# Performance work log

Measured on AMD Instinct MI355X. Metric: run time of the kernel, lower is better.

Reference implementation:

```python
import jax, jax.numpy as jnp
import numpy as np
from jax import lax

B, S, H, E, K = 2, 1024, 2048, 16, 4
CAP = int(B * S * 1.5 * K / E)  # capacity = 768
ALPHA = 0.7

def _mlp2(x, w1, b1, w2, b2):
    return jnp.maximum(x @ w1 + b1, 0.0) @ w2 + b2

def setup_inputs() -> dict:
    key = jax.random.key(0)
    ks = iter(jax.random.split(key, 32))
    def w(shape, scale=0.02):
        return (jax.random.normal(next(ks), shape, dtype=jnp.float32) * scale)
    inp = {
        'hidden_states': jax.random.normal(next(ks), (B, S, H), dtype=jnp.float32),
        'mod_image': jax.random.normal(next(ks), (B, S, H), dtype=jnp.float32),
        'mod_genomic': jax.random.normal(next(ks), (B, S, H), dtype=jnp.float32),
        'g_w1': w((H, H)), 'g_b1': jnp.zeros((H,), jnp.float32),
        'g_w2': w((H, E)), 'g_b2': jnp.zeros((E,), jnp.float32),
        'm_w1': w((H, H)), 'm_b1': jnp.zeros((H,), jnp.float32),
        'm_w2': w((H, H)), 'm_b2': jnp.zeros((H,), jnp.float32),
    }
    for p in ('si', 'sg', 'sc', 'sb'):
        inp[p + '_w1'] = w((H, H // 2)); inp[p + '_b1'] = jnp.zeros((H // 2,), jnp.float32)
        inp[p + '_w2'] = w((H // 2, E)); inp[p + '_b2'] = jnp.zeros((E,), jnp.float32)
    return inp

def reference(hidden_states, mod_image, mod_genomic,
              g_w1, g_b1, g_w2, g_b2,
              si_w1, si_b1, si_w2, si_b2,
              sg_w1, sg_b1, sg_w2, sg_b2,
              sc_w1, sc_b1, sc_w2, sc_b2,
              sb_w1, sb_b1, sb_w2, sb_b2,
              m_w1, m_b1, m_w2, m_b2):
    # generalized router probs over experts
    g_probs = jax.nn.softmax(_mlp2(hidden_states, g_w1, g_b1, g_w2, g_b2), axis=-1)
    # missing-modality representation (clinical + biospecimen are missing)
    miss = _mlp2(hidden_states, m_w1, m_b1, m_w2, m_b2)
    # specialized routers: image, genomic (available) + clinical, biospecimen (use miss)
    s_probs = (jax.nn.softmax(_mlp2(mod_image, si_w1, si_b1, si_w2, si_b2), axis=-1)
               + jax.nn.softmax(_mlp2(mod_genomic, sg_w1, sg_b1, sg_w2, sg_b2), axis=-1)
               + jax.nn.softmax(_mlp2(miss, sc_w1, sc_b1, sc_w2, sc_b2), axis=-1)
               + jax.nn.softmax(_mlp2(miss, sb_w1, sb_b1, sb_w2, sb_b2), axis=-1))
    s_probs = s_probs / 2.0  # divided by len(available_modalities) == 2, as in source
    router_probs = ALPHA * g_probs + (1.0 - ALPHA) * s_probs  # [B,S,E]
    top_k_probs, top_k_idx = lax.top_k(router_probs, K)  # [B,S,K]
    top_k_probs = top_k_probs / top_k_probs.sum(axis=-1, keepdims=True)
    onehot = jax.nn.one_hot(top_k_idx, E, dtype=router_probs.dtype)  # [B,S,K,E]
    dmask = onehot.sum(axis=-2)                               # [B,S,E] (0/1: experts distinct)
    cmask = (onehot * top_k_probs[..., None]).sum(axis=-2)    # [B,S,E]
    dispatch = jnp.zeros((B, S, E, CAP), router_probs.dtype).at[..., 0].set(dmask)
    combine = jnp.zeros((B, S, E, CAP), router_probs.dtype).at[..., 0].set(cmask)
    mean_probs = router_probs.mean(axis=(0, 1))  # [E]
    aux_loss = jnp.sum(mean_probs * jnp.log(mean_probs * E + 1e-9))
    return dispatch, combine, router_probs, aux_loss
```

## Files before the change

kernel.cpp:

```cpp
#include <hip/hip_runtime.h>
#include <math.h>
#include <stdint.h>

#define NTOK 2048
#define HDIM 2048
#define HHALF 1024
#define EDIM 16
#define CAPV 768
#define TOPK 4

typedef __bf16 bf16x8 __attribute__((ext_vector_type(8)));
typedef __bf16 bf16x4 __attribute__((ext_vector_type(4)));
typedef float f32x4 __attribute__((ext_vector_type(4)));


#define GK 2048
#define BKT 64

struct GJob {
  const __bf16* Ah; const __bf16* Al;
  const __bf16* Wh; const __bf16* Wl;
  const float* bias;
  float* Cf;
  __bf16* Ch; __bf16* Cl;
  int relu; int N; int blk0;
};
struct GJobs { GJob j[4]; int njobs; };

__device__ __forceinline__ void stage_tile(const __bf16* __restrict__ g,
                                           int grow0, int k0,
                                           __bf16* lbase, int wid, int lane) {
  int r_in = lane >> 3;
  int swz_elems = ((lane & 7) ^ r_in) << 3;
#pragma unroll
  for (int i = 0; i < 4; ++i) {
    int row0 = wid * 32 + i * 8;
    const __bf16* src = g + (size_t)(grow0 + row0 + r_in) * GK + k0 + swz_elems;
    __builtin_amdgcn_global_load_lds(
        (const __attribute__((address_space(1))) uint32_t*)src,
        (__attribute__((address_space(3))) uint32_t*)(lbase + row0 * BKT),
        16, 0, 0);
  }
}

__global__ __launch_bounds__(256) void gemm_split(GJobs P) {
  __shared__ __align__(16) __bf16 lds[4 * 128 * BKT];
  __bf16* ldsAh = lds;
  __bf16* ldsAl = lds + 8192;
  __bf16* ldsBh = lds + 16384;
  __bf16* ldsBl = lds + 24576;
  const char* cAh = (const char*)ldsAh;
  const char* cAl = (const char*)ldsAl;
  const char* cBh = (const char*)ldsBh;
  const char* cBl = (const char*)ldsBl;

  const int bid = blockIdx.x;
  int ji = 0;
#pragma unroll
  for (int k = 1; k < 4; ++k)
    if (k < P.njobs && bid >= P.j[k].blk0) ji = k;
  const GJob J = P.j[ji];
  const int local = bid - J.blk0;
  const int nbx = J.N >> 7;
  const int bx = local & (nbx - 1);
  const int by = local / nbx;
  const int m0 = by * 128;
  const int n0 = bx * 128;

  const int tid = threadIdx.x;
  const int wid = tid >> 6;
  const int lane = tid & 63;
  const int lane15 = lane & 15;
  const int c0 = lane >> 4;
  const int wr = wid >> 1;
  const int wc = wid & 1;

  int offA[4][2], offB[4][2];
#pragma unroll
  for (int i = 0; i < 4; ++i) {
    int ra = wr * 64 + i * 16 + lane15;
    int rb = wc * 64 + i * 16 + lane15;
#pragma unroll
    for (int ks = 0; ks < 2; ++ks) {
      offA[i][ks] = ra * 128 + (((ks * 4 + c0) ^ (ra & 7)) << 4);
      offB[i][ks] = rb * 128 + (((ks * 4 + c0) ^ (rb & 7)) << 4);
    }
  }

  f32x4 acc[4][4];
#pragma unroll
  for (int i = 0; i < 4; ++i)
#pragma unroll
    for (int j = 0; j < 4; ++j) acc[i][j] = (f32x4){0.f, 0.f, 0.f, 0.f};

  for (int k0 = 0; k0 < GK; k0 += BKT) {
    stage_tile(J.Ah, m0, k0, ldsAh, wid, lane);
    stage_tile(J.Al, m0, k0, ldsAl, wid, lane);
    stage_tile(J.Wh, n0, k0, ldsBh, wid, lane);
    stage_tile(J.Wl, n0, k0, ldsBl, wid, lane);
    __syncthreads();
#pragma unroll
    for (int ks = 0; ks < 2; ++ks) {
      bf16x8 ah[4], al[4], bh[4], bl[4];
#pragma unroll
      for (int i = 0; i < 4; ++i) {
        ah[i] = *(const bf16x8*)(cAh + offA[i][ks]);
        al[i] = *(const bf16x8*)(cAl + offA[i][ks]);
        bh[i] = *(const bf16x8*)(cBh + offB[i][ks]);
        bl[i] = *(const bf16x8*)(cBl + offB[i][ks]);
      }
#pragma unroll
      for (int mi = 0; mi < 4; ++mi)
#pragma unroll
        for (int ni = 0; ni < 4; ++ni) {
          acc[mi][ni] = __builtin_amdgcn_mfma_f32_16x16x32_bf16(
              ah[mi], bh[ni], acc[mi][ni], 0, 0, 0);
          acc[mi][ni] = __builtin_amdgcn_mfma_f32_16x16x32_bf16(
              ah[mi], bl[ni], acc[mi][ni], 0, 0, 0);
          acc[mi][ni] = __builtin_amdgcn_mfma_f32_16x16x32_bf16(
              al[mi], bh[ni], acc[mi][ni], 0, 0, 0);
        }
    }
    __syncthreads();
  }

#pragma unroll
  for (int mi = 0; mi < 4; ++mi) {
#pragma unroll
    for (int ni = 0; ni < 4; ++ni) {
      int col = n0 + wc * 64 + ni * 16 + lane15;
      float bv = J.bias[col];
      f32x4 v = acc[mi][ni];
#pragma unroll
      for (int j = 0; j < 4; ++j) {
        int row = m0 + wr * 64 + mi * 16 + c0 * 4 + j;
        float x = v[j] + bv;
        if (J.relu) x = fmaxf(x, 0.0f);
        size_t o = (size_t)row * J.N + col;
        if (J.Cf) J.Cf[o] = x;
        if (J.Ch) {
          __bf16 hh = (__bf16)x;
          J.Ch[o] = hh;
          J.Cl[o] = (__bf16)(x - (float)hh);
        }
      }
    }
  }
}

struct SJob { const float* in; __bf16* h; __bf16* l; };
#define SPLIT_BLKS 4096
__global__ __launch_bounds__(256) void split3(SJob a, SJob b, SJob c) {
  int job = blockIdx.x >> 12;
  SJob J = (job == 0) ? a : (job == 1) ? b : c;
  int i = (blockIdx.x & 4095) * 256 + threadIdx.x;
  float4 v = ((const float4*)J.in)[i];
  bf16x4 hv, lv;
  hv.x = (__bf16)v.x; lv.x = (__bf16)(v.x - (float)hv.x);
  hv.y = (__bf16)v.y; lv.y = (__bf16)(v.y - (float)hv.y);
  hv.z = (__bf16)v.z; lv.z = (__bf16)(v.z - (float)hv.z);
  hv.w = (__bf16)v.w; lv.w = (__bf16)(v.w - (float)hv.w);
  ((bf16x4*)J.h)[i] = hv;
  ((bf16x4*)J.l)[i] = lv;
}

struct TJob { const float* W; __bf16* Th; __bf16* Tl; int Nd; };
struct TJobs { TJob j[7]; };
__global__ __launch_bounds__(256) void tsplit(TJobs P) {
  const TJob J = P.j[blockIdx.z];
  int n0 = blockIdx.x * 32;
  if (n0 >= J.Nd) return;
  int k0 = blockIdx.y * 32;
  __shared__ float t[32][33];
  int tx = threadIdx.x & 31, ty = threadIdx.x >> 5;
#pragma unroll
  for (int i = 0; i < 4; ++i) {
    int kk = ty + i * 8;
    t[kk][tx] = J.W[(size_t)(k0 + kk) * J.Nd + n0 + tx];
  }
  __syncthreads();
#pragma unroll
  for (int i = 0; i < 4; ++i) {
    int nn = ty + i * 8;
    float v = t[tx][nn];
    __bf16 hh = (__bf16)v;
    size_t o = (size_t)(n0 + nn) * GK + k0 + tx;
    J.Th[o] = hh;
    J.Tl[o] = (__bf16)(v - (float)hh);
  }
}

struct LJob { const float* Y; const float* W2; const float* b2; float* L; int K; };
struct LJobs { LJob j[5]; };
__global__ __launch_bounds__(256) void logits_kernel(LJobs P) {
  const LJob J = P.j[blockIdx.x >> 8];
  const int blk = blockIdx.x & 255;
  const int tid = threadIdx.x;
  const int wid = tid >> 6, lane = tid & 63;
  const int e = lane & 15;
  const int kq = lane >> 4;
  const int tok0 = blk * 8 + wid * 2;
  const float* y0 = J.Y + (size_t)tok0 * J.K;
  const float* y1 = y0 + J.K;
  const int KQ = J.K >> 2;
  const int kbase = kq * KQ;
  float a0 = 0.f, a1 = 0.f;
#pragma unroll 8
  for (int k = 0; k < KQ; ++k) {
    int kk = kbase + k;
    float w = J.W2[(size_t)kk * EDIM + e];
    a0 = fmaf(y0[kk], w, a0);
    a1 = fmaf(y1[kk], w, a1);
  }
  a0 += __shfl_xor(a0, 16); a0 += __shfl_xor(a0, 32);
  a1 += __shfl_xor(a1, 16); a1 += __shfl_xor(a1, 32);
  if (lane < 16) {
    float b = J.b2[e];
    J.L[(size_t)tok0 * EDIM + e] = a0 + b;
    J.L[(size_t)(tok0 + 1) * EDIM + e] = a1 + b;
  }
}

__device__ __forceinline__ void softmax16(const float* __restrict__ L, float* __restrict__ p) {
  float v[16];
  *(float4*)&v[0]  = *(const float4*)&L[0];
  *(float4*)&v[4]  = *(const float4*)&L[4];
  *(float4*)&v[8]  = *(const float4*)&L[8];
  *(float4*)&v[12] = *(const float4*)&L[12];
  float m = v[0];
#pragma unroll
  for (int e = 1; e < 16; ++e) m = fmaxf(m, v[e]);
  float s = 0.0f;
#pragma unroll
  for (int e = 0; e < 16; ++e) { v[e] = expf(v[e] - m); s += v[e]; }
  float inv = 1.0f / s;
#pragma unroll
  for (int e = 0; e < 16; ++e) p[e] = v[e] * inv;
}

__global__ __launch_bounds__(256) void finalize_kernel(
    const float* __restrict__ Lg, const float* __restrict__ Lsi,
    const float* __restrict__ Lsg, const float* __restrict__ Lsc,
    const float* __restrict__ Lsb,
    float* __restrict__ dispatch, float* __restrict__ combine,
    float* __restrict__ router_probs, float* __restrict__ mean_acc) {
  __shared__ float sm[EDIM];
  int tid = threadIdx.x;
  if (tid < EDIM) sm[tid] = 0.0f;
  __syncthreads();

  int tok = blockIdx.x * 256 + tid;
  float pg[16], ps[16], tmp[16], r[16];
  softmax16(Lg + (size_t)tok * EDIM, pg);
  softmax16(Lsi + (size_t)tok * EDIM, ps);
  softmax16(Lsg + (size_t)tok * EDIM, tmp);
#pragma unroll
  for (int e = 0; e < 16; ++e) ps[e] += tmp[e];
  softmax16(Lsc + (size_t)tok * EDIM, tmp);
#pragma unroll
  for (int e = 0; e < 16; ++e) ps[e] += tmp[e];
  softmax16(Lsb + (size_t)tok * EDIM, tmp);
#pragma unroll
  for (int e = 0; e < 16; ++e) ps[e] += tmp[e];

#pragma unroll
  for (int e = 0; e < 16; ++e) {
    float s = ps[e] * 0.5f;
    r[e] = 0.7f * pg[e] + 0.3f * s;
  }

#pragma unroll
  for (int e = 0; e < 16; e += 4) {
    float4 o = {r[e], r[e + 1], r[e + 2], r[e + 3]};
    *(float4*)&router_probs[(size_t)tok * EDIM + e] = o;
  }

#pragma unroll
  for (int e = 0; e < 16; ++e) atomicAdd(&sm[e], r[e]);

  bool used[16];
#pragma unroll
  for (int e = 0; e < 16; ++e) used[e] = false;
  int idx[TOPK];
  float tp[TOPK];
  float tsum = 0.0f;
#pragma unroll
  for (int j = 0; j < TOPK; ++j) {
    float best = -1.0f;
    int bi = 0;
#pragma unroll
    for (int e = 0; e < 16; ++e) {
      bool take = (!used[e]) && (r[e] > best);
      best = take ? r[e] : best;
      bi = take ? e : bi;
    }
    used[bi] = true;
    idx[j] = bi;
    tp[j] = best;
    tsum += best;
  }
  float invt = 1.0f / tsum;
#pragma unroll
  for (int j = 0; j < TOPK; ++j) {
    size_t off = ((size_t)tok * EDIM + idx[j]) * CAPV;
    dispatch[off] = 1.0f;
    combine[off] = tp[j] * invt;
  }

  __syncthreads();
  if (tid < EDIM) atomicAdd(&mean_acc[tid], sm[tid]);
}

__global__ void aux_kernel(const float* __restrict__ mean_acc, float* __restrict__ out_aux) {
  if (threadIdx.x == 0 && blockIdx.x == 0) {
    float s = 0.0f;
    for (int e = 0; e < EDIM; ++e) {
      float m = mean_acc[e] * (1.0f / (float)NTOK);
      s += m * logf(m * (float)EDIM + 1e-9f);
    }
    *out_aux = s;
  }
}

#define MBYTE (1ull << 20)

extern "C" void kernel_launch(void* const* d_in, const int* in_sizes, int n_in,
                              void* d_out, int out_size, void* d_ws, size_t ws_size,
                              hipStream_t stream) {
  const float* X    = (const float*)d_in[0];
  const float* IMG  = (const float*)d_in[1];
  const float* GEN  = (const float*)d_in[2];
  const float* g_w1 = (const float*)d_in[3];
  const float* g_b1 = (const float*)d_in[4];
  const float* g_w2 = (const float*)d_in[5];
  const float* g_b2 = (const float*)d_in[6];
  const float* m_w1 = (const float*)d_in[7];
  const float* m_b1 = (const float*)d_in[8];
  const float* m_w2 = (const float*)d_in[9];
  const float* m_b2 = (const float*)d_in[10];
  const float* si_w1 = (const float*)d_in[11];
  const float* si_b1 = (const float*)d_in[12];
  const float* si_w2 = (const float*)d_in[13];
  const float* si_b2 = (const float*)d_in[14];
  const float* sg_w1 = (const float*)d_in[15];
  const float* sg_b1 = (const float*)d_in[16];
  const float* sg_w2 = (const float*)d_in[17];
  const float* sg_b2 = (const float*)d_in[18];
  const float* sc_w1 = (const float*)d_in[19];
  const float* sc_b1 = (const float*)d_in[20];
  const float* sc_w2 = (const float*)d_in[21];
  const float* sc_b2 = (const float*)d_in[22];
  const float* sb_w1 = (const float*)d_in[23];
  const float* sb_b1 = (const float*)d_in[24];
  const float* sb_w2 = (const float*)d_in[25];
  const float* sb_b2 = (const float*)d_in[26];

  char* wsb = (char*)d_ws;
  __bf16* Xh   = (__bf16*)(wsb + 0 * MBYTE);
  __bf16* Xl   = (__bf16*)(wsb + 8 * MBYTE);
  __bf16* IMGh = (__bf16*)(wsb + 16 * MBYTE);
  __bf16* IMGl = (__bf16*)(wsb + 24 * MBYTE);
  __bf16* GENh = (__bf16*)(wsb + 32 * MBYTE);
  __bf16* GENl = (__bf16*)(wsb + 40 * MBYTE);
  __bf16* Wmw1h = (__bf16*)(wsb + 48 * MBYTE);
  __bf16* Wmw1l = (__bf16*)(wsb + 56 * MBYTE);
  __bf16* Wgw1h = (__bf16*)(wsb + 64 * MBYTE);
  __bf16* Wgw1l = (__bf16*)(wsb + 72 * MBYTE);
  __bf16* Wmw2h = (__bf16*)(wsb + 80 * MBYTE);
  __bf16* Wmw2l = (__bf16*)(wsb + 88 * MBYTE);
  __bf16* Wsch = (__bf16*)(wsb + 96 * MBYTE);
  __bf16* Wscl = (__bf16*)(wsb + 104 * MBYTE);
  __bf16* Wsbh = (__bf16*)(wsb + 112 * MBYTE);
  __bf16* Wsbl = (__bf16*)(wsb + 120 * MBYTE);
  __bf16* Wsih = (__bf16*)(wsb + 128 * MBYTE);
  __bf16* Wsil = (__bf16*)(wsb + 136 * MBYTE);
  __bf16* Wsgh = (__bf16*)(wsb + 144 * MBYTE);
  __bf16* Wsgl = (__bf16*)(wsb + 152 * MBYTE);
  __bf16* H1h  = (__bf16*)(wsb + 160 * MBYTE);
  __bf16* H1l  = (__bf16*)(wsb + 168 * MBYTE);
  __bf16* MISSh = (__bf16*)(wsb + 176 * MBYTE);
  __bf16* MISSl = (__bf16*)(wsb + 184 * MBYTE);
  float*  YG  = (float*)(wsb + 192 * MBYTE);
  float*  YSC = (float*)(wsb + 208 * MBYTE);
  float*  YSB = (float*)(wsb + 216 * MBYTE);
  float*  YSI = (float*)(wsb + 224 * MBYTE);
  float*  YSG = (float*)(wsb + 232 * MBYTE);
  float* L0 = (float*)(wsb + 240 * MBYTE);
  float* L1 = L0 + NTOK * EDIM;
  float* L2 = L1 + NTOK * EDIM;
  float* L3 = L2 + NTOK * EDIM;
  float* L4 = L3 + NTOK * EDIM;
  float* meanp = L4 + NTOK * EDIM;

  float* dispatch = (float*)d_out;
  float* combine = dispatch + (size_t)NTOK * EDIM * CAPV;
  float* rp = combine + (size_t)NTOK * EDIM * CAPV;
  float* aux = rp + (size_t)NTOK * EDIM;

  hipMemsetAsync(d_out, 0, (size_t)out_size * sizeof(float), stream);
  hipMemsetAsync(meanp, 0, EDIM * sizeof(float), stream);

  dim3 blk(256);

  {
    SJob a{X, Xh, Xl}, b{IMG, IMGh, IMGl}, c{GEN, GENh, GENl};
    split3<<<3 * SPLIT_BLKS, blk, 0, stream>>>(a, b, c);
  }

  {
    TJobs t;
    t.j[0] = {m_w1, Wmw1h, Wmw1l, HDIM};
    t.j[1] = {g_w1, Wgw1h, Wgw1l, HDIM};
    t.j[2] = {m_w2, Wmw2h, Wmw2l, HDIM};
    t.j[3] = {sc_w1, Wsch, Wscl, HHALF};
    t.j[4] = {sb_w1, Wsbh, Wsbl, HHALF};
    t.j[5] = {si_w1, Wsih, Wsil, HHALF};
    t.j[6] = {sg_w1, Wsgh, Wsgl, HHALF};
    tsplit<<<dim3(64, 64, 7), blk, 0, stream>>>(t);
  }

  {
    GJobs g;
    g.j[0] = {Xh, Xl, Wmw1h, Wmw1l, m_b1, nullptr, H1h, H1l, 1, HDIM, 0};
    g.j[1] = {Xh, Xl, Wgw1h, Wgw1l, g_b1, YG, nullptr, nullptr, 1, HDIM, 256};
    g.j[2] = {IMGh, IMGl, Wsih, Wsil, si_b1, YSI, nullptr, nullptr, 1, HHALF, 512};
    g.j[3] = {GENh, GENl, Wsgh, Wsgl, sg_b1, YSG, nullptr, nullptr, 1, HHALF, 640};
    g.njobs = 4;
    gemm_split<<<768, blk, 0, stream>>>(g);
  }

  {
    GJobs g;
    g.j[0] = {H1h, H1l, Wmw2h, Wmw2l, m_b2, nullptr, MISSh, MISSl, 0, HDIM, 0};
    g.njobs = 1;
    gemm_split<<<256, blk, 0, stream>>>(g);
  }

  {
    GJobs g;
    g.j[0] = {MISSh, MISSl, Wsch, Wscl, sc_b1, YSC, nullptr, nullptr, 1, HHALF, 0};
    g.j[1] = {MISSh, MISSl, Wsbh, Wsbl, sb_b1, YSB, nullptr, nullptr, 1, HHALF, 128};
    g.njobs = 2;
    gemm_split<<<256, blk, 0, stream>>>(g);
  }

  {
    LJobs l;
    l.j[0] = {YG, g_w2, g_b2, L0, HDIM};
    l.j[1] = {YSI, si_w2, si_b2, L1, HHALF};
    l.j[2] = {YSG, sg_w2, sg_b2, L2, HHALF};
    l.j[3] = {YSC, sc_w2, sc_b2, L3, HHALF};
    l.j[4] = {YSB, sb_w2, sb_b2, L4, HHALF};
    logits_kernel<<<5 * 256, blk, 0, stream>>>(l);
  }

  finalize_kernel<<<NTOK / 256, blk, 0, stream>>>(L0, L1, L2, L3, L4,
                                                  dispatch, combine, rp, meanp);
  aux_kernel<<<1, 64, 0, stream>>>(meanp, aux);
}
```

Baseline: 487.3 us.

## Fold missing-modality second layer into router weights and use larger-tile GEMM

The code precomputes the products of the sc/sb router first-layer weights with m_w2 (weight-only GEMMs), plus the matching folded biases, so the missing-modality output MISS is never materialized. The dependent stage H1→MISS→YSC/YSB becomes H1→YSC/YSB, which removes one full 2048×2048×2048 split-precision GEMM from the token path. The first-layer GEMMs and the weight-fold GEMMs all run in one new 512-thread, 256×256-tile kernel with double-buffered direct-to-LDS loads. In exchange there is extra weight-only GEMM work, the rounding changes because the folded weights are re-split into bf16 hi/lo, and the launch is a single wave of 256 large blocks.

```diff
diff --git a/kernel.cpp b/kernel.cpp
--- a/kernel.cpp
+++ b/kernel.cpp
@@ -8,13 +8,170 @@
 #define EDIM 16
 #define CAPV 768
 #define TOPK 4
+#define GK 2048
 
 typedef __bf16 bf16x8 __attribute__((ext_vector_type(8)));
 typedef __bf16 bf16x4 __attribute__((ext_vector_type(4)));
 typedef float f32x4 __attribute__((ext_vector_type(4)));
 
 
-#define GK 2048
+struct GJobA {
+  const __bf16 *Ah, *Al, *Wh, *Wl;
+  const float* bias;
+  float* Cf; __bf16 *Ch, *Cl;
+  int relu, N, blk0;
+};
+struct GJobsA { GJobA j[6]; };
+
+#define BKA 32
+#define NTA 64
+
+__global__ __launch_bounds__(512, 2) void gemm_bigA(GJobsA P) {
+  __shared__ __align__(16) __bf16 lds[2][4][256 * BKA];
+
+  const int tid = threadIdx.x;
+  const int wid = tid >> 6, lane = tid & 63;
+  const int lane15 = lane & 15, c0 = lane >> 4;
+
+  const int bid = blockIdx.x;
+  int ji = 0;
+#pragma unroll
+  for (int k = 1; k < 6; ++k)
+    if (bid >= P.j[k].blk0) ji = k;
+  const GJobA J = P.j[ji];
+  const int local = bid - J.blk0;
+  const int nbx = J.N >> 8;
+  const int bx = local & (nbx - 1);
+  const int by = local / nbx;
+  const int m0 = by * 256, n0 = bx * 256;
+
+  const int wr = wid >> 2, wc = wid & 3;
+
+  int srow[2], soff[2];
+#pragma unroll
+  for (int h = 0; h < 2; ++h) {
+    int s = tid + h * 512;
+    int row = s >> 2;
+    srow[h] = row;
+    soff[h] = ((s & 3) ^ ((row >> 1) & 3)) * 8;
+  }
+
+  int offB[4], offA[2][4];
+#pragma unroll
+  for (int ni = 0; ni < 4; ++ni) {
+    int rb = wc * 64 + ni * 16 + lane15;
+    offB[ni] = rb * 64 + ((c0 ^ ((rb >> 1) & 3)) << 4);
+  }
+#pragma unroll
+  for (int mh = 0; mh < 2; ++mh)
+#pragma unroll
+    for (int i = 0; i < 4; ++i) {
+      int ra = wr * 128 + mh * 64 + i * 16 + lane15;
+      offA[mh][i] = ra * 64 + ((c0 ^ ((ra >> 1) & 3)) << 4);
+    }
+
+#define STAGE_ARR(gptr, grow0, k0, larr)                                       \
+  {                                                                            \
+    _Pragma("unroll") for (int h = 0; h < 2; ++h) {                            \
+      const __bf16* _src =                                                     \
+          (gptr) + (size_t)((grow0) + srow[h]) * GK + (k0) + soff[h];          \
+      __builtin_amdgcn_global_load_lds(                                        \
+          (const __attribute__((address_space(1))) uint32_t*)_src,             \
+          (__attribute__((address_space(3))) uint32_t*)((larr) +               \
+                                                        (wid * 64 + h * 512) * 8), \
+          16, 0, 0);                                                           \
+    }                                                                          \
+  }
+
+#define STAGE_TILE(buf, k0)                                                    \
+  {                                                                            \
+    STAGE_ARR(J.Ah, m0, (k0), lds[buf][0]);                                    \
+    STAGE_ARR(J.Al, m0, (k0), lds[buf][1]);                                    \
+    STAGE_ARR(J.Wh, n0, (k0), lds[buf][2]);                                    \
+    STAGE_ARR(J.Wl, n0, (k0), lds[buf][3]);                                    \
+  }
+
+  f32x4 acc[8][4];
+#pragma unroll
+  for (int i = 0; i < 8; ++i)
+#pragma unroll
+    for (int j = 0; j < 4; ++j) acc[i][j] = (f32x4){0.f, 0.f, 0.f, 0.f};
+
+  STAGE_TILE(0, 0);
+
+  for (int t = 0; t < NTA; ++t) {
+    const int cur = t & 1;
+    if (t + 1 < NTA) {
+      STAGE_TILE(cur ^ 1, (t + 1) * BKA);
+      asm volatile("s_waitcnt vmcnt(8)" ::: "memory");
+    } else {
+      asm volatile("s_waitcnt vmcnt(0)" ::: "memory");
+    }
+    __builtin_amdgcn_s_barrier();
+    __builtin_amdgcn_sched_barrier(0);
+
+    const char* cAh = (const char*)lds[cur][0];
+    const char* cAl = (const char*)lds[cur][1];
+    const char* cBh = (const char*)lds[cur][2];
+    const char* cBl = (const char*)lds[cur][3];
+
+    bf16x8 bh[4], bl[4];
+#pragma unroll
+    for (int ni = 0; ni < 4; ++ni) {
+      bh[ni] = *(const bf16x8*)(cBh + offB[ni]);
+      bl[ni] = *(const bf16x8*)(cBl + offB[ni]);
+    }
+#pragma unroll
+    for (int mh = 0; mh < 2; ++mh) {
+      bf16x8 ah[4], al[4];
+#pragma unroll
+      for (int i = 0; i < 4; ++i) {
+        ah[i] = *(const bf16x8*)(cAh + offA[mh][i]);
+        al[i] = *(const bf16x8*)(cAl + offA[mh][i]);
+      }
+#pragma unroll
+      for (int mi = 0; mi < 4; ++mi)
+#pragma unroll
+        for (int ni = 0; ni < 4; ++ni) {
+          acc[mh * 4 + mi][ni] = __builtin_amdgcn_mfma_f32_16x16x32_bf16(
+              ah[mi], bh[ni], acc[mh * 4 + mi][ni], 0, 0, 0);
+          acc[mh * 4 + mi][ni] = __builtin_amdgcn_mfma_f32_16x16x32_bf16(
+              ah[mi], bl[ni], acc[mh * 4 + mi][ni], 0, 0, 0);
+          acc[mh * 4 + mi][ni] = __builtin_amdgcn_mfma_f32_16x16x32_bf16(
+              al[mi], bh[ni], acc[mh * 4 + mi][ni], 0, 0, 0);
+        }
+    }
+    __builtin_amdgcn_sched_barrier(0);
+    __builtin_amdgcn_s_barrier();
+  }
+
+#pragma unroll
+  for (int mh = 0; mh < 2; ++mh)
+#pragma unroll
+    for (int mi = 0; mi < 4; ++mi)
+#pragma unroll
+      for (int ni = 0; ni < 4; ++ni) {
+        int col = n0 + wc * 64 + ni * 16 + lane15;
+        float bv = J.bias[col];
+        f32x4 v = acc[mh * 4 + mi][ni];
+#pragma unroll
+        for (int j = 0; j < 4; ++j) {
+          int row = m0 + wr * 128 + mh * 64 + mi * 16 + c0 * 4 + j;
+          float x = v[j] + bv;
+          if (J.relu) x = fmaxf(x, 0.0f);
+          size_t o = (size_t)row * J.N + col;
+          if (J.Cf) J.Cf[o] = x;
+          if (J.Ch) {
+            __bf16 hh = (__bf16)x;
+            J.Ch[o] = hh;
+            J.Cl[o] = (__bf16)(x - (float)hh);
+          }
+        }
+      }
+#undef STAGE_ARR
+#undef STAGE_TILE
+}
+
 #define BKT 64
 
 struct GJob {
@@ -150,9 +307,9 @@
 
 struct SJob { const float* in; __bf16* h; __bf16* l; };
 #define SPLIT_BLKS 4096
-__global__ __launch_bounds__(256) void split3(SJob a, SJob b, SJob c) {
+__global__ __launch_bounds__(256) void split4(SJob a, SJob b, SJob c, SJob d) {
   int job = blockIdx.x >> 12;
-  SJob J = (job == 0) ? a : (job == 1) ? b : c;
+  SJob J = (job == 0) ? a : (job == 1) ? b : (job == 2) ? c : d;
   int i = (blockIdx.x & 4095) * 256 + threadIdx.x;
   float4 v = ((const float4*)J.in)[i];
   bf16x4 hv, lv;
@@ -165,7 +322,7 @@
 }
 
 struct TJob { const float* W; __bf16* Th; __bf16* Tl; int Nd; };
-struct TJobs { TJob j[7]; };
+struct TJobs { TJob j[6]; };
 __global__ __launch_bounds__(256) void tsplit(TJobs P) {
   const TJob J = P.j[blockIdx.z];
   int n0 = blockIdx.x * 32;
@@ -188,6 +345,20 @@
     J.Th[o] = hh;
     J.Tl[o] = (__bf16)(v - (float)hh);
   }
+}
+
+__global__ __launch_bounds__(256) void prebias(
+    const float* __restrict__ b2,
+    const float* __restrict__ W1a, const float* __restrict__ b1a, float* va,
+    const float* __restrict__ W1b, const float* __restrict__ b1b, float* vb) {
+  const float* W1 = blockIdx.y ? W1b : W1a;
+  const float* b1 = blockIdx.y ? b1b : b1a;
+  float* v = blockIdx.y ? vb : va;
+  int n = blockIdx.x * 256 + threadIdx.x;
+  float acc = b1[n];
+#pragma unroll 8
+  for (int k = 0; k < GK; ++k) acc = fmaf(b2[k], W1[(size_t)k * HHALF + n], acc);
+  v[n] = acc;
 }
 
 struct LJob { const float* Y; const float* W2; const float* b2; float* L; int K; };
@@ -356,41 +527,46 @@
   const float* sb_b2 = (const float*)d_in[26];
 
   char* wsb = (char*)d_ws;
-  __bf16* Xh   = (__bf16*)(wsb + 0 * MBYTE);
-  __bf16* Xl   = (__bf16*)(wsb + 8 * MBYTE);
-  __bf16* IMGh = (__bf16*)(wsb + 16 * MBYTE);
-  __bf16* IMGl = (__bf16*)(wsb + 24 * MBYTE);
-  __bf16* GENh = (__bf16*)(wsb + 32 * MBYTE);
-  __bf16* GENl = (__bf16*)(wsb + 40 * MBYTE);
-  __bf16* Wmw1h = (__bf16*)(wsb + 48 * MBYTE);
-  __bf16* Wmw1l = (__bf16*)(wsb + 56 * MBYTE);
-  __bf16* Wgw1h = (__bf16*)(wsb + 64 * MBYTE);
-  __bf16* Wgw1l = (__bf16*)(wsb + 72 * MBYTE);
-  __bf16* Wmw2h = (__bf16*)(wsb + 80 * MBYTE);
-  __bf16* Wmw2l = (__bf16*)(wsb + 88 * MBYTE);
-  __bf16* Wsch = (__bf16*)(wsb + 96 * MBYTE);
-  __bf16* Wscl = (__bf16*)(wsb + 104 * MBYTE);
-  __bf16* Wsbh = (__bf16*)(wsb + 112 * MBYTE);
-  __bf16* Wsbl = (__bf16*)(wsb + 120 * MBYTE);
-  __bf16* Wsih = (__bf16*)(wsb + 128 * MBYTE);
-  __bf16* Wsil = (__bf16*)(wsb + 136 * MBYTE);
-  __bf16* Wsgh = (__bf16*)(wsb + 144 * MBYTE);
-  __bf16* Wsgl = (__bf16*)(wsb + 152 * MBYTE);
-  __bf16* H1h  = (__bf16*)(wsb + 160 * MBYTE);
-  __bf16* H1l  = (__bf16*)(wsb + 168 * MBYTE);
-  __bf16* MISSh = (__bf16*)(wsb + 176 * MBYTE);
-  __bf16* MISSl = (__bf16*)(wsb + 184 * MBYTE);
-  float*  YG  = (float*)(wsb + 192 * MBYTE);
-  float*  YSC = (float*)(wsb + 208 * MBYTE);
-  float*  YSB = (float*)(wsb + 216 * MBYTE);
-  float*  YSI = (float*)(wsb + 224 * MBYTE);
-  float*  YSG = (float*)(wsb + 232 * MBYTE);
-  float* L0 = (float*)(wsb + 240 * MBYTE);
+  __bf16* Xh    = (__bf16*)(wsb + 0 * MBYTE);
+  __bf16* Xl    = (__bf16*)(wsb + 8 * MBYTE);
+  __bf16* IMGh  = (__bf16*)(wsb + 16 * MBYTE);
+  __bf16* IMGl  = (__bf16*)(wsb + 24 * MBYTE);
+  __bf16* GENh  = (__bf16*)(wsb + 32 * MBYTE);
+  __bf16* GENl  = (__bf16*)(wsb + 40 * MBYTE);
+  __bf16* M2h   = (__bf16*)(wsb + 48 * MBYTE);
+  __bf16* M2l   = (__bf16*)(wsb + 56 * MBYTE);
+  __bf16* Wm1h  = (__bf16*)(wsb + 64 * MBYTE);
+  __bf16* Wm1l  = (__bf16*)(wsb + 72 * MBYTE);
+  __bf16* Wg1h  = (__bf16*)(wsb + 80 * MBYTE);
+  __bf16* Wg1l  = (__bf16*)(wsb + 88 * MBYTE);
+  __bf16* Wsch  = (__bf16*)(wsb + 96 * MBYTE);
+  __bf16* Wscl  = (__bf16*)(wsb + 100 * MBYTE);
+  __bf16* Wsbh  = (__bf16*)(wsb + 104 * MBYTE);
+  __bf16* Wsbl  = (__bf16*)(wsb + 108 * MBYTE);
+  __bf16* Wsih  = (__bf16*)(wsb + 112 * MBYTE);
+  __bf16* Wsil  = (__bf16*)(wsb + 116 * MBYTE);
+  __bf16* Wsgh  = (__bf16*)(wsb + 120 * MBYTE);
+  __bf16* Wsgl  = (__bf16*)(wsb + 124 * MBYTE);
+  __bf16* H1h   = (__bf16*)(wsb + 128 * MBYTE);
+  __bf16* H1l   = (__bf16*)(wsb + 136 * MBYTE);
+  __bf16* WPsch = (__bf16*)(wsb + 144 * MBYTE);
+  __bf16* WPscl = (__bf16*)(wsb + 148 * MBYTE);
+  __bf16* WPsbh = (__bf16*)(wsb + 152 * MBYTE);
+  __bf16* WPsbl = (__bf16*)(wsb + 156 * MBYTE);
+  float*  YG    = (float*)(wsb + 160 * MBYTE);
+  float*  YSI   = (float*)(wsb + 176 * MBYTE);
+  float*  YSG   = (float*)(wsb + 184 * MBYTE);
+  float*  YSC   = (float*)(wsb + 192 * MBYTE);
+  float*  YSB   = (float*)(wsb + 200 * MBYTE);
+  float* L0 = (float*)(wsb + 208 * MBYTE);
   float* L1 = L0 + NTOK * EDIM;
   float* L2 = L1 + NTOK * EDIM;
   float* L3 = L2 + NTOK * EDIM;
   float* L4 = L3 + NTOK * EDIM;
   float* meanp = L4 + NTOK * EDIM;
+  float* zbias = meanp + EDIM;
+  float* vsc = zbias + GK;
+  float* vsb = vsc + HHALF;
 
   float* dispatch = (float*)d_out;
   float* combine = dispatch + (size_t)NTOK * EDIM * CAPV;
@@ -398,48 +574,44 @@
   float* aux = rp + (size_t)NTOK * EDIM;
 
   hipMemsetAsync(d_out, 0, (size_t)out_size * sizeof(float), stream);
-  hipMemsetAsync(meanp, 0, EDIM * sizeof(float), stream);
+  hipMemsetAsync(meanp, 0, (EDIM + GK) * sizeof(float), stream);
 
   dim3 blk(256);
 
   {
-    SJob a{X, Xh, Xl}, b{IMG, IMGh, IMGl}, c{GEN, GENh, GENl};
-    split3<<<3 * SPLIT_BLKS, blk, 0, stream>>>(a, b, c);
+    SJob a{X, Xh, Xl}, b{IMG, IMGh, IMGl}, c{GEN, GENh, GENl}, d{m_w2, M2h, M2l};
+    split4<<<4 * SPLIT_BLKS, blk, 0, stream>>>(a, b, c, d);
   }
 
   {
     TJobs t;
-    t.j[0] = {m_w1, Wmw1h, Wmw1l, HDIM};
-    t.j[1] = {g_w1, Wgw1h, Wgw1l, HDIM};
-    t.j[2] = {m_w2, Wmw2h, Wmw2l, HDIM};
-    t.j[3] = {sc_w1, Wsch, Wscl, HHALF};
-    t.j[4] = {sb_w1, Wsbh, Wsbl, HHALF};
-    t.j[5] = {si_w1, Wsih, Wsil, HHALF};
-    t.j[6] = {sg_w1, Wsgh, Wsgl, HHALF};
-    tsplit<<<dim3(64, 64, 7), blk, 0, stream>>>(t);
+    t.j[0] = {m_w1, Wm1h, Wm1l, HDIM};
+    t.j[1] = {g_w1, Wg1h, Wg1l, HDIM};
+    t.j[2] = {sc_w1, Wsch, Wscl, HHALF};
+    t.j[3] = {sb_w1, Wsbh, Wsbl, HHALF};
+    t.j[4] = {si_w1, Wsih, Wsil, HHALF};
+    t.j[5] = {sg_w1, Wsgh, Wsgl, HHALF};
+    tsplit<<<dim3(64, 64, 6), blk, 0, stream>>>(t);
+  }
+
+  prebias<<<dim3(HHALF / 256, 2), blk, 0, stream>>>(m_b2, sc_w1, sc_b1, vsc,
+                                                    sb_w1, sb_b1, vsb);
+
+  {
+    GJobsA g;
+    g.j[0] = {Xh, Xl, Wm1h, Wm1l, m_b1, nullptr, H1h, H1l, 1, HDIM, 0};
+    g.j[1] = {Xh, Xl, Wg1h, Wg1l, g_b1, YG, nullptr, nullptr, 1, HDIM, 64};
+    g.j[2] = {IMGh, IMGl, Wsih, Wsil, si_b1, YSI, nullptr, nullptr, 1, HHALF, 128};
+    g.j[3] = {GENh, GENl, Wsgh, Wsgl, sg_b1, YSG, nullptr, nullptr, 1, HHALF, 160};
+    g.j[4] = {Wsch, Wscl, M2h, M2l, zbias, nullptr, WPsch, WPscl, 0, HDIM, 192};
+    g.j[5] = {Wsbh, Wsbl, M2h, M2l, zbias, nullptr, WPsbh, WPsbl, 0, HDIM, 224};
+    gemm_bigA<<<256, dim3(512), 0, stream>>>(g);
   }
 
   {
     GJobs g;
-    g.j[0] = {Xh, Xl, Wmw1h, Wmw1l, m_b1, nullptr, H1h, H1l, 1, HDIM, 0};
-    g.j[1] = {Xh, Xl, Wgw1h, Wgw1l, g_b1, YG, nullptr, nullptr, 1, HDIM, 256};
-    g.j[2] = {IMGh, IMGl, Wsih, Wsil, si_b1, YSI, nullptr, nullptr, 1, HHALF, 512};
-    g.j[3] = {GENh, GENl, Wsgh, Wsgl, sg_b1, YSG, nullptr, nullptr, 1, HHALF, 640};
-    g.njobs = 4;
-    gemm_split<<<768, blk, 0, stream>>>(g);
-  }
-
-  {
-    GJobs g;
-    g.j[0] = {H1h, H1l, Wmw2h, Wmw2l, m_b2, nullptr, MISSh, MISSl, 0, HDIM, 0};
-    g.njobs = 1;
-    gemm_split<<<256, blk, 0, stream>>>(g);
-  }
-
-  {
-    GJobs g;
-    g.j[0] = {MISSh, MISSl, Wsch, Wscl, sc_b1, YSC, nullptr, nullptr, 1, HHALF, 0};
-    g.j[1] = {MISSh, MISSl, Wsbh, Wsbl, sb_b1, YSB, nullptr, nullptr, 1, HHALF, 128};
+    g.j[0] = {H1h, H1l, WPsch, WPscl, vsc, YSC, nullptr, nullptr, 1, HHALF, 0};
+    g.j[1] = {H1h, H1l, WPsbh, WPsbl, vsb, YSB, nullptr, nullptr, 1, HHALF, 128};
     g.njobs = 2;
     gemm_split<<<256, blk, 0, stream>>>(g);
   }
```

New measurement: 517.4 us. 1.06x slower.
